# Kernel optimization log

Measured on AMD Instinct MI355X. Metric: run time of the kernel, lower is better.

## Reference

```python
import jax, jax.numpy as jnp
import numpy as np

N_NODES = 50000
N_EDGES = 800000
DIM_IN = 64
DIM_HID = 128
DIM_OUT = 64


def _linear_init(key, fan_in, fan_out):
    # torch nn.Linear default: U(-1/sqrt(fan_in), 1/sqrt(fan_in)) for W and b
    kw, kb = jax.random.split(key)
    bound = 1.0 / np.sqrt(fan_in)
    W = jax.random.uniform(kw, (fan_in, fan_out), minval=-bound, maxval=bound, dtype=jnp.float32)
    b = jax.random.uniform(kb, (fan_out,), minval=-bound, maxval=bound, dtype=jnp.float32)
    return W, b


def setup_inputs() -> dict:
    key = jax.random.key(0)
    kx, ke, k0, k1, k2 = jax.random.split(key, 5)
    x = jax.random.normal(kx, (N_NODES, DIM_IN), dtype=jnp.float32)
    edge_idx = jax.random.randint(ke, (2, N_EDGES), 0, N_NODES, dtype=jnp.int64)
    W0, b0 = _linear_init(k0, 2 * DIM_IN, DIM_HID)
    W1, b1 = _linear_init(k1, DIM_HID, DIM_HID)
    W2, b2 = _linear_init(k2, DIM_HID, DIM_OUT)
    return {"x": x, "edge_idx": edge_idx, "W0": W0, "b0": b0,
            "W1": W1, "b1": b1, "W2": W2, "b2": b2}


def reference(x, edge_idx, W0, b0, W1, b1, W2, b2):
    row, col = edge_idx[0], edge_idx[1]
    # gather + concat edge features: [E, 2*dim_in]
    h = jnp.concatenate([x[row], x[col]], axis=-1)
    h = jax.nn.softplus(h @ W0 + b0)
    h = jax.nn.softplus(h @ W1 + b1)
    h = h @ W2 + b2  # [E, dim_out]
    # scatter-add edge messages to source nodes
    return jax.ops.segment_sum(h, row, num_segments=x.shape[0])
```

## Files before the change

### kernel.cpp

```cpp
#include <hip/hip_runtime.h>
#include <math.h>

#define N_NODES 50000
#define N_EDGES 800000
#define DIM_IN 64
#define DIM_HID 128
#define DIM_OUT 64
#define WROW 128
#define NTILES (N_EDGES / 32)
#define GRID 512
#define NWAVES (GRID * 8)

typedef __attribute__((ext_vector_type(8))) short short8;
typedef __attribute__((ext_vector_type(4))) float f32x4;

union U8 { uint4 u; short8 s; };

__device__ __forceinline__ unsigned short f2bf(float f) {
    unsigned u = __float_as_uint(f);
    return (unsigned short)((u + 0x7fffu + ((u >> 16) & 1u)) >> 16);
}

__device__ __forceinline__ unsigned cvt_pk_bf16(float a, float b) {
    unsigned d;
    asm("v_cvt_pk_bf16_f32 %0, %1, %2" : "=v"(d) : "v"(a), "v"(b));
    return d;
}

__device__ __forceinline__ float exp2_fast(float a) {
#if __has_builtin(__builtin_amdgcn_exp2f)
    return __builtin_amdgcn_exp2f(a);
#else
    return __expf(a * 0.69314718f);
#endif
}

__device__ __forceinline__ unsigned sp2(float x0, float x1) {
    const float L2E = 1.44269504f;
    float z0 = exp2_fast(-fabsf(x0) * L2E);
    float z1 = exp2_fast(-fabsf(x1) * L2E);
    float p0 = fmaf(fmaf(fmaf(-0.1011458f, z0, 0.2942925f), z0, -0.5f), z0, 1.0f) * z0;
    float p1 = fmaf(fmaf(fmaf(-0.1011458f, z1, 0.2942925f), z1, -0.5f), z1, 1.0f) * z1;
    return cvt_pk_bf16(fmaxf(x0, 0.0f) + p0, fmaxf(x1, 0.0f) + p1);
}

template <bool DO_XBF>
__global__ void prep_all(const float* __restrict__ x,
                         const float* __restrict__ W0,
                         const float* __restrict__ W1,
                         const float* __restrict__ W2,
                         unsigned short* __restrict__ wt,
                         unsigned short* __restrict__ xbf) {
    int i = blockIdx.x * blockDim.x + threadIdx.x;

    if (DO_XBF && i < (N_NODES * DIM_IN / 4)) {
        float4 v = *((const float4*)x + i);
        uint2 p;
        p.x = cvt_pk_bf16(v.x, v.y);
        p.y = cvt_pk_bf16(v.z, v.w);
        *((uint2*)xbf + i) = p;
    }

    if (i < 320 * WROW) {
        int row = i >> 7, s = i & 127;
        float v;
        int f = ((s >> 5) << 5) | (((s & 7) >> 2) << 4) | (((s >> 3) & 3) << 2) | (s & 3);
        if (row < 128)      v = W0[s * DIM_HID + row];
        else if (row < 256) v = W1[f * DIM_HID + (row - 128)];
        else                v = W2[f * DIM_OUT + (row - 256)];
        wt[i] = f2bf(v);
    }
}

template <bool XB>
__global__ __launch_bounds__(512, 4)
void edge_mlp_mfma(const float* __restrict__ x,
                   const unsigned short* __restrict__ xbf,
                   const int* __restrict__ eidx,
                   const unsigned short* __restrict__ wt,
                   const float* __restrict__ b0,
                   const float* __restrict__ b1,
                   const float* __restrict__ b2,
                   float* __restrict__ out) {
    __shared__ unsigned short lw[256 * WROW];

    const int lane = threadIdx.x & 63;
    const int w    = threadIdx.x >> 6;
    const int l16  = lane & 15;
    const int q    = lane >> 4;
    const int sx   = l16 & 7;
    const int gwid = blockIdx.x * 8 + w;

    {
        const uint4* src = (const uint4*)wt;
        uint4* dst = (uint4*)lw;
#pragma unroll
        for (int it = 0; it < 8; ++it) {
            int i = threadIdx.x + it * 512;
            int row = i >> 4, col = i & 15;
            dst[(row << 4) | (col ^ (row & 7))] = src[i];
        }
    }
    __syncthreads();

    const unsigned short* Wt2 = wt + 256 * WROW;

    auto load_tile = [&](int t, int (&nsv)[8], short8 (&h)[2][4]) {
        const int e0 = t * 32;
        int nR[2], nC[2];
#pragma unroll
        for (int m = 0; m < 2; ++m) {
            nR[m] = eidx[e0 + m * 16 + l16];
            nC[m] = eidx[N_EDGES + e0 + m * 16 + l16];
        }
#pragma unroll
        for (int m = 0; m < 2; ++m)
#pragma unroll
            for (int r = 0; r < 4; ++r)
                nsv[m * 4 + r] = eidx[e0 + m * 16 + q * 4 + r];
#pragma unroll
        for (int m = 0; m < 2; ++m)
#pragma unroll
            for (int kk = 0; kk < 4; ++kk) {
                int node = (kk >= 2) ? nC[m] : nR[m];
                if (XB) {
                    h[m][kk] = *(const short8*)(xbf + (size_t)node * DIM_IN + (kk & 1) * 32 + q * 8);
                } else {
                    const float* p = x + (size_t)node * DIM_IN + (kk & 1) * 32 + q * 8;
                    float4 v0 = *(const float4*)p;
                    float4 v1 = *(const float4*)(p + 4);
                    U8 tt;
                    tt.u.x = cvt_pk_bf16(v0.x, v0.y);
                    tt.u.y = cvt_pk_bf16(v0.z, v0.w);
                    tt.u.z = cvt_pk_bf16(v1.x, v1.y);
                    tt.u.w = cvt_pk_bf16(v1.z, v1.w);
                    h[m][kk] = tt.s;
                }
            }
    };

    int tile = gwid;
    int ns[8];
    short8 hfr[2][4];
    load_tile(tile, ns, hfr);

    while (true) {
#pragma unroll
        for (int L = 0; L < 2; ++L) {
            const float* bias = L ? b1 : b0;
            unsigned d[2][8][2];
#pragma unroll
            for (int ti = 0; ti < 8; ++ti) {
                f32x4 bb = *(const f32x4*)(bias + ti * 16 + q * 4);
                f32x4 a0 = bb, a1 = bb;
                const unsigned short* rowb = lw + ((L * 128 + ti * 16 + l16) * WROW);
                short8 wf[4];
#pragma unroll
                for (int kk = 0; kk < 4; ++kk)
                    wf[kk] = *(const short8*)(rowb + ((kk * 4 + q) ^ sx) * 8);
#pragma unroll
                for (int kk = 0; kk < 4; ++kk) {
                    a0 = __builtin_amdgcn_mfma_f32_16x16x32_bf16(wf[kk], hfr[0][kk], a0, 0, 0, 0);
                    a1 = __builtin_amdgcn_mfma_f32_16x16x32_bf16(wf[kk], hfr[1][kk], a1, 0, 0, 0);
                }
                d[0][ti][0] = sp2(a0[0], a0[1]);
                d[0][ti][1] = sp2(a0[2], a0[3]);
                d[1][ti][0] = sp2(a1[0], a1[1]);
                d[1][ti][1] = sp2(a1[2], a1[3]);
            }
#pragma unroll
            for (int m = 0; m < 2; ++m)
#pragma unroll
                for (int kk = 0; kk < 4; ++kk) {
                    U8 t;
                    t.u.x = d[m][2 * kk][0];
                    t.u.y = d[m][2 * kk][1];
                    t.u.z = d[m][2 * kk + 1][0];
                    t.u.w = d[m][2 * kk + 1][1];
                    hfr[m][kk] = t.s;
                }
        }

        f32x4 acc[4][2];
#pragma unroll
        for (int ti = 0; ti < 4; ++ti) {
            float bv = b2[ti * 16 + l16];
            f32x4 a0 = (f32x4){bv, bv, bv, bv};
            f32x4 a1 = a0;
            const unsigned short* Wp = Wt2 + (ti * 16 + l16) * WROW + q * 8;
            short8 wf[4];
#pragma unroll
            for (int kk = 0; kk < 4; ++kk)
                wf[kk] = *(const short8*)(Wp + kk * 32);
#pragma unroll
            for (int kk = 0; kk < 4; ++kk) {
                a0 = __builtin_amdgcn_mfma_f32_16x16x32_bf16(hfr[0][kk], wf[kk], a0, 0, 0, 0);
                a1 = __builtin_amdgcn_mfma_f32_16x16x32_bf16(hfr[1][kk], wf[kk], a1, 0, 0, 0);
            }
            acc[ti][0] = a0;
            acc[ti][1] = a1;
        }

        const int nxt = tile + NWAVES;
        const bool more = (nxt < NTILES);
        int ns2[8];
        short8 hfr2[2][4];
        if (more) load_tile(nxt, ns2, hfr2);

#pragma unroll
        for (int ti = 0; ti < 4; ++ti)
#pragma unroll
            for (int r = 0; r < 4; ++r) {
                atomicAdd(out + (size_t)ns[r] * DIM_OUT + ti * 16 + l16, acc[ti][0][r]);
                atomicAdd(out + (size_t)ns[4 + r] * DIM_OUT + ti * 16 + l16, acc[ti][1][r]);
            }

        if (!more) break;
        tile = nxt;
#pragma unroll
        for (int i = 0; i < 8; ++i) ns[i] = ns2[i];
#pragma unroll
        for (int m = 0; m < 2; ++m)
#pragma unroll
            for (int kk = 0; kk < 4; ++kk)
                hfr[m][kk] = hfr2[m][kk];
    }
}

extern "C" void kernel_launch(void* const* d_in, const int* in_sizes, int n_in,
                              void* d_out, int out_size, void* d_ws, size_t ws_size,
                              hipStream_t stream) {
    const float* x  = (const float*)d_in[0];
    const int*   ei = (const int*)d_in[1];
    const float* W0 = (const float*)d_in[2];
    const float* b0 = (const float*)d_in[3];
    const float* W1 = (const float*)d_in[4];
    const float* b1 = (const float*)d_in[5];
    const float* W2 = (const float*)d_in[6];
    const float* b2 = (const float*)d_in[7];
    float* out = (float*)d_out;

    unsigned short* wt = (unsigned short*)d_ws;
    const size_t WT_BYTES = (size_t)320 * WROW * sizeof(unsigned short);
    unsigned short* xbf = (unsigned short*)((char*)d_ws + WT_BYTES);
    const size_t need = WT_BYTES + (size_t)N_NODES * DIM_IN * sizeof(unsigned short);

    hipMemsetAsync(out, 0, (size_t)N_NODES * DIM_OUT * sizeof(float), stream);

    if (ws_size >= need) {
        prep_all<true><<<(N_NODES * DIM_IN / 4 + 255) / 256, 256, 0, stream>>>(
            x, W0, W1, W2, wt, xbf);
        edge_mlp_mfma<true><<<GRID, 512, 0, stream>>>(
            x, xbf, ei, wt, b0, b1, b2, out);
    } else {
        prep_all<false><<<(320 * WROW + 255) / 256, 256, 0, stream>>>(
            x, W0, W1, W2, wt, nullptr);
        edge_mlp_mfma<false><<<GRID, 512, 0, stream>>>(
            x, nullptr, ei, wt, b0, b1, b2, out);
    }
}
```

Baseline: 313.3 us.

## Remove software prefetch of next edge tile and relax launch bounds

Drops the double-buffered load of the next tile's edge indices and gathered node features, so each iteration loads and computes its tile serially inside a plain strided loop. It also lowers the minimum blocks-per-CU hint in launch_bounds from 4 to 2, which lets the compiler use more registers per thread. The aim is to cut register pressure and copy overhead from the prefetch buffers. The cost is that gather latency is no longer overlapped with the atomic scatter and must be hidden by other waves instead, and occupancy may fall if register use grows.

```diff
diff --git a/kernel.cpp b/kernel.cpp
--- a/kernel.cpp
+++ b/kernel.cpp
@@ -73,7 +73,7 @@
 }
 
 template <bool XB>
-__global__ __launch_bounds__(512, 4)
+__global__ __launch_bounds__(512, 2)
 void edge_mlp_mfma(const float* __restrict__ x,
                    const unsigned short* __restrict__ xbf,
                    const int* __restrict__ eidx,
@@ -105,46 +105,43 @@
 
     const unsigned short* Wt2 = wt + 256 * WROW;
 
-    auto load_tile = [&](int t, int (&nsv)[8], short8 (&h)[2][4]) {
-        const int e0 = t * 32;
-        int nR[2], nC[2];
+    for (int tile = gwid; tile < NTILES; tile += NWAVES) {
+        const int e0 = tile * 32;
+
+        int nodeR[2], nodeC[2];
 #pragma unroll
         for (int m = 0; m < 2; ++m) {
-            nR[m] = eidx[e0 + m * 16 + l16];
-            nC[m] = eidx[N_EDGES + e0 + m * 16 + l16];
-        }
+            nodeR[m] = eidx[e0 + m * 16 + l16];
+            nodeC[m] = eidx[N_EDGES + e0 + m * 16 + l16];
+        }
+        int ns[8];
 #pragma unroll
         for (int m = 0; m < 2; ++m)
 #pragma unroll
             for (int r = 0; r < 4; ++r)
-                nsv[m * 4 + r] = eidx[e0 + m * 16 + q * 4 + r];
+                ns[m * 4 + r] = eidx[e0 + m * 16 + q * 4 + r];
+
+        short8 hfr[2][4];
 #pragma unroll
         for (int m = 0; m < 2; ++m)
 #pragma unroll
             for (int kk = 0; kk < 4; ++kk) {
-                int node = (kk >= 2) ? nC[m] : nR[m];
+                int node = (kk >= 2) ? nodeC[m] : nodeR[m];
                 if (XB) {
-                    h[m][kk] = *(const short8*)(xbf + (size_t)node * DIM_IN + (kk & 1) * 32 + q * 8);
+                    hfr[m][kk] = *(const short8*)(xbf + (size_t)node * DIM_IN + (kk & 1) * 32 + q * 8);
                 } else {
                     const float* p = x + (size_t)node * DIM_IN + (kk & 1) * 32 + q * 8;
                     float4 v0 = *(const float4*)p;
                     float4 v1 = *(const float4*)(p + 4);
-                    U8 tt;
-                    tt.u.x = cvt_pk_bf16(v0.x, v0.y);
-                    tt.u.y = cvt_pk_bf16(v0.z, v0.w);
-                    tt.u.z = cvt_pk_bf16(v1.x, v1.y);
-                    tt.u.w = cvt_pk_bf16(v1.z, v1.w);
-                    h[m][kk] = tt.s;
+                    U8 t;
+                    t.u.x = cvt_pk_bf16(v0.x, v0.y);
+                    t.u.y = cvt_pk_bf16(v0.z, v0.w);
+                    t.u.z = cvt_pk_bf16(v1.x, v1.y);
+                    t.u.w = cvt_pk_bf16(v1.z, v1.w);
+                    hfr[m][kk] = t.s;
                 }
             }
-    };
-
-    int tile = gwid;
-    int ns[8];
-    short8 hfr[2][4];
-    load_tile(tile, ns, hfr);
-
-    while (true) {
+
 #pragma unroll
         for (int L = 0; L < 2; ++L) {
             const float* bias = L ? b1 : b0;
@@ -201,12 +198,6 @@
             acc[ti][1] = a1;
         }
 
-        const int nxt = tile + NWAVES;
-        const bool more = (nxt < NTILES);
-        int ns2[8];
-        short8 hfr2[2][4];
-        if (more) load_tile(nxt, ns2, hfr2);
-
 #pragma unroll
         for (int ti = 0; ti < 4; ++ti)
 #pragma unroll
@@ -214,16 +205,6 @@
                 atomicAdd(out + (size_t)ns[r] * DIM_OUT + ti * 16 + l16, acc[ti][0][r]);
                 atomicAdd(out + (size_t)ns[4 + r] * DIM_OUT + ti * 16 + l16, acc[ti][1][r]);
             }
-
-        if (!more) break;
-        tile = nxt;
-#pragma unroll
-        for (int i = 0; i < 8; ++i) ns[i] = ns2[i];
-#pragma unroll
-        for (int m = 0; m < 2; ++m)
-#pragma unroll
-            for (int kk = 0; kk < 4; ++kk)
-                hfr[m][kk] = hfr2[m][kk];
     }
 }
 
```

Result: faster. 281.9 us (-10.0%).

## Rebalance LDS: keep W0 and W2 plus biases in shared, read W1 from global

Applied to the files above, without the earlier changes.

Layer 1 weights now come from global memory/cache, while W0, W2 and all biases sit in LDS. This shrinks the block's LDS footprint from 64KB to about 49KB. The launch-bounds minimum occupancy drops from 4 to 2, giving the compiler more registers. The destination node indices for the scatter are now loaded late, right before the atomics, instead of being prefetched a tile ahead. W1 reads go through the L1/L2 path, unswizzled, and may add latency to the hottest layer.

```diff
diff --git a/kernel.cpp b/kernel.cpp
--- a/kernel.cpp
+++ b/kernel.cpp
@@ -73,7 +73,7 @@
 }
 
 template <bool XB>
-__global__ __launch_bounds__(512, 4)
+__global__ __launch_bounds__(512, 2)
 void edge_mlp_mfma(const float* __restrict__ x,
                    const unsigned short* __restrict__ xbf,
                    const int* __restrict__ eidx,
@@ -82,7 +82,9 @@
                    const float* __restrict__ b1,
                    const float* __restrict__ b2,
                    float* __restrict__ out) {
-    __shared__ unsigned short lw[256 * WROW];
+    __shared__ unsigned short lw0[128 * WROW];
+    __shared__ unsigned short lw2[64 * WROW];
+    __shared__ float lb[128 + 128 + 64];
 
     const int lane = threadIdx.x & 63;
     const int w    = threadIdx.x >> 6;
@@ -92,32 +94,32 @@
     const int gwid = blockIdx.x * 8 + w;
 
     {
-        const uint4* src = (const uint4*)wt;
-        uint4* dst = (uint4*)lw;
-#pragma unroll
-        for (int it = 0; it < 8; ++it) {
+        const uint4* s0 = (const uint4*)wt;
+        uint4* d0 = (uint4*)lw0;
+#pragma unroll
+        for (int it = 0; it < 4; ++it) {
             int i = threadIdx.x + it * 512;
             int row = i >> 4, col = i & 15;
-            dst[(row << 4) | (col ^ (row & 7))] = src[i];
-        }
+            d0[(row << 4) | (col ^ (row & 7))] = s0[i];
+        }
+        const uint4* s2 = (const uint4*)(wt + 256 * WROW);
+        uint4* d2 = (uint4*)lw2;
+#pragma unroll
+        for (int it = 0; it < 2; ++it) {
+            int i = threadIdx.x + it * 512;
+            int row = i >> 4, col = i & 15;
+            d2[(row << 4) | (col ^ (row & 7))] = s2[i];
+        }
+        int t = threadIdx.x;
+        if (t < 128)      lb[t] = b0[t];
+        else if (t < 256) lb[t] = b1[t - 128];
+        else if (t < 320) lb[t] = b2[t - 256];
     }
     __syncthreads();
 
-    const unsigned short* Wt2 = wt + 256 * WROW;
-
-    auto load_tile = [&](int t, int (&nsv)[8], short8 (&h)[2][4]) {
-        const int e0 = t * 32;
-        int nR[2], nC[2];
-#pragma unroll
-        for (int m = 0; m < 2; ++m) {
-            nR[m] = eidx[e0 + m * 16 + l16];
-            nC[m] = eidx[N_EDGES + e0 + m * 16 + l16];
-        }
-#pragma unroll
-        for (int m = 0; m < 2; ++m)
-#pragma unroll
-            for (int r = 0; r < 4; ++r)
-                nsv[m * 4 + r] = eidx[e0 + m * 16 + q * 4 + r];
+    const unsigned short* Wt1 = wt + 128 * WROW;
+
+    auto gather = [&](int e0, const int (&nR)[2], const int (&nC)[2], short8 (&h)[2][4]) {
 #pragma unroll
         for (int m = 0; m < 2; ++m)
 #pragma unroll
@@ -129,35 +131,49 @@
                     const float* p = x + (size_t)node * DIM_IN + (kk & 1) * 32 + q * 8;
                     float4 v0 = *(const float4*)p;
                     float4 v1 = *(const float4*)(p + 4);
-                    U8 tt;
-                    tt.u.x = cvt_pk_bf16(v0.x, v0.y);
-                    tt.u.y = cvt_pk_bf16(v0.z, v0.w);
-                    tt.u.z = cvt_pk_bf16(v1.x, v1.y);
-                    tt.u.w = cvt_pk_bf16(v1.z, v1.w);
-                    h[m][kk] = tt.s;
+                    U8 t;
+                    t.u.x = cvt_pk_bf16(v0.x, v0.y);
+                    t.u.y = cvt_pk_bf16(v0.z, v0.w);
+                    t.u.z = cvt_pk_bf16(v1.x, v1.y);
+                    t.u.w = cvt_pk_bf16(v1.z, v1.w);
+                    h[m][kk] = t.s;
                 }
             }
     };
 
     int tile = gwid;
-    int ns[8];
     short8 hfr[2][4];
-    load_tile(tile, ns, hfr);
+    {
+        const int e0 = tile * 32;
+        int nR[2], nC[2];
+#pragma unroll
+        for (int m = 0; m < 2; ++m) {
+            nR[m] = eidx[e0 + m * 16 + l16];
+            nC[m] = eidx[N_EDGES + e0 + m * 16 + l16];
+        }
+        gather(e0, nR, nC, hfr);
+    }
 
     while (true) {
 #pragma unroll
         for (int L = 0; L < 2; ++L) {
-            const float* bias = L ? b1 : b0;
             unsigned d[2][8][2];
 #pragma unroll
             for (int ti = 0; ti < 8; ++ti) {
-                f32x4 bb = *(const f32x4*)(bias + ti * 16 + q * 4);
+                f32x4 bb = *(const f32x4*)(lb + L * 128 + ti * 16 + q * 4);
                 f32x4 a0 = bb, a1 = bb;
-                const unsigned short* rowb = lw + ((L * 128 + ti * 16 + l16) * WROW);
                 short8 wf[4];
-#pragma unroll
-                for (int kk = 0; kk < 4; ++kk)
-                    wf[kk] = *(const short8*)(rowb + ((kk * 4 + q) ^ sx) * 8);
+                if (L == 0) {
+                    const unsigned short* rowb = lw0 + (ti * 16 + l16) * WROW;
+#pragma unroll
+                    for (int kk = 0; kk < 4; ++kk)
+                        wf[kk] = *(const short8*)(rowb + ((kk * 4 + q) ^ sx) * 8);
+                } else {
+                    const unsigned short* Wp = Wt1 + (ti * 16 + l16) * WROW + q * 8;
+#pragma unroll
+                    for (int kk = 0; kk < 4; ++kk)
+                        wf[kk] = *(const short8*)(Wp + kk * 32);
+                }
 #pragma unroll
                 for (int kk = 0; kk < 4; ++kk) {
                     a0 = __builtin_amdgcn_mfma_f32_16x16x32_bf16(wf[kk], hfr[0][kk], a0, 0, 0, 0);
@@ -184,14 +200,14 @@
         f32x4 acc[4][2];
 #pragma unroll
         for (int ti = 0; ti < 4; ++ti) {
-            float bv = b2[ti * 16 + l16];
+            float bv = lb[256 + ti * 16 + l16];
             f32x4 a0 = (f32x4){bv, bv, bv, bv};
             f32x4 a1 = a0;
-            const unsigned short* Wp = Wt2 + (ti * 16 + l16) * WROW + q * 8;
+            const unsigned short* rowb = lw2 + (ti * 16 + l16) * WROW;
             short8 wf[4];
 #pragma unroll
             for (int kk = 0; kk < 4; ++kk)
-                wf[kk] = *(const short8*)(Wp + kk * 32);
+                wf[kk] = *(const short8*)(rowb + ((kk * 4 + q) ^ sx) * 8);
 #pragma unroll
             for (int kk = 0; kk < 4; ++kk) {
                 a0 = __builtin_amdgcn_mfma_f32_16x16x32_bf16(hfr[0][kk], wf[kk], a0, 0, 0, 0);
@@ -203,9 +219,26 @@
 
         const int nxt = tile + NWAVES;
         const bool more = (nxt < NTILES);
-        int ns2[8];
+        const int e0c = tile * 32;
+
+        int nR2[2], nC2[2];
+        if (more) {
+            const int e0n = nxt * 32;
+#pragma unroll
+            for (int m = 0; m < 2; ++m) {
+                nR2[m] = eidx[e0n + m * 16 + l16];
+                nC2[m] = eidx[N_EDGES + e0n + m * 16 + l16];
+            }
+        }
+        int ns[8];
+#pragma unroll
+        for (int m = 0; m < 2; ++m)
+#pragma unroll
+            for (int r = 0; r < 4; ++r)
+                ns[m * 4 + r] = eidx[e0c + m * 16 + q * 4 + r];
+
         short8 hfr2[2][4];
-        if (more) load_tile(nxt, ns2, hfr2);
+        if (more) gather(nxt * 32, nR2, nC2, hfr2);
 
 #pragma unroll
         for (int ti = 0; ti < 4; ++ti)
@@ -217,8 +250,6 @@
 
         if (!more) break;
         tile = nxt;
-#pragma unroll
-        for (int i = 0; i < 8; ++i) ns[i] = ns2[i];
 #pragma unroll
         for (int m = 0; m < 2; ++m)
 #pragma unroll
```

Measured after the change: 272.7 us. 1.15x faster.
